# Performance work log

Measured on AMD Instinct MI355X. Metric: run time of the kernel, lower is better.

The kernel has to match this reference:

```python
import jax, jax.numpy as jnp
import numpy as np

B, M, E, R = 4, 72, 24, 552          # docs, mentions/doc, entities/doc, pairs/doc
L, H, A = 1024, 1024, 16             # seq_len, hidden (LUKE-large), attn heads
EMB, BLK, OUT, NC = 768, 64, 768, 97 # embed_size, block_size, out_embed_size, num_class


def setup_inputs() -> dict:
    key = jax.random.key(0)
    ks = jax.random.split(key, 12)
    s = 0.02  # weight scale to keep tanh unsaturated
    return {
        "seq_lhs": jax.random.normal(ks[0], (B, L, H), jnp.float32),
        "ent_lhs": jax.random.normal(ks[1], (B, M, H), jnp.float32),
        "ent_to_seq_attn": jax.random.uniform(ks[2], (B, A, M, L), jnp.float32),
        "entity_id_labels": jax.random.randint(ks[3], (B, M), 0, E, jnp.int32),
        "hts": jax.random.randint(ks[4], (B, R, 2), 0, E, jnp.int32),
        "W_head": jax.random.normal(ks[5], (2 * H, EMB), jnp.float32) * s,
        "b_head": jnp.zeros((EMB,), jnp.float32),
        "W_tail": jax.random.normal(ks[6], (2 * H, EMB), jnp.float32) * s,
        "b_tail": jnp.zeros((EMB,), jnp.float32),
        "W_bil": jax.random.normal(ks[7], (EMB * BLK, OUT), jnp.float32) * s,
        "b_bil": jnp.zeros((OUT,), jnp.float32),
        "W_cls": jax.random.normal(ks[8], (OUT, NC), jnp.float32) * s,
        "b_cls": jnp.zeros((NC,), jnp.float32),
        "W_bin": jax.random.normal(ks[9], (OUT, 1), jnp.float32) * s,
        "b_bin": jnp.zeros((1,), jnp.float32),
    }


def _hrt_pool(seq_lhs, ent_lhs, ent_to_seq_attn, entity_id_labels, hts):
    # global segment id: doc_i * E + entity_label  -> [B*M]
    seg = (jnp.arange(B, dtype=entity_id_labels.dtype)[:, None] * E
           + entity_id_labels).reshape(-1)
    NSEG = B * E

    # --- entity embedding: logsumexp over mentions of each entity (0 if empty) ---
    x = ent_lhs.reshape(B * M, H)
    mx = jax.ops.segment_max(x, seg, num_segments=NSEG)          # -inf for empty
    mx_safe = jnp.where(jnp.isfinite(mx), mx, 0.0)
    ssum = jax.ops.segment_sum(jnp.exp(x - mx_safe[seg]), seg, num_segments=NSEG)
    cnt = jax.ops.segment_sum(jnp.ones((B * M,), x.dtype), seg, num_segments=NSEG)
    ent_emb = jnp.where(cnt[:, None] > 0, jnp.log(ssum) + mx_safe, 0.0)
    ent_emb = ent_emb.reshape(B, E, H)

    # --- entity-to-seq attention: mean over mentions (0 if empty) ---
    a = ent_to_seq_attn.transpose(0, 2, 1, 3).reshape(B * M, A, L)
    asum = jax.ops.segment_sum(a, seg, num_segments=NSEG)
    amean = jnp.where(cnt[:, None, None] > 0,
                      asum / jnp.maximum(cnt, 1.0)[:, None, None], 0.0)
    amean = amean.reshape(B, E, A, L)

    # --- gather head/tail per pair ---
    bidx = jnp.arange(B)[:, None]
    hs = ent_emb[bidx, hts[:, :, 0]]       # [B,R,H]
    ts = ent_emb[bidx, hts[:, :, 1]]
    ha = amean[bidx, hts[:, :, 0]]         # [B,R,A,L]
    ta = amean[bidx, hts[:, :, 1]]

    ht_attn = (ha * ta).mean(axis=2)       # [B,R,L] mean over heads
    ht_attn = ht_attn / (ht_attn.sum(axis=-1, keepdims=True) + 1e-5)
    rel = jnp.einsum('bld,brl->brd', seq_lhs, ht_attn)  # [B,R,H]
    return hs, ts, rel


def reference(seq_lhs, ent_lhs, ent_to_seq_attn, entity_id_labels, hts,
              W_head, b_head, W_tail, b_tail, W_bil, b_bil,
              W_cls, b_cls, W_bin, b_bin):
    hs, ts, rel = _hrt_pool(seq_lhs, ent_lhs, ent_to_seq_attn,
                            entity_id_labels, hts)
    N = B * R
    hs = jnp.tanh(jnp.concatenate([hs, rel], -1).reshape(N, 2 * H) @ W_head + b_head)
    ts = jnp.tanh(jnp.concatenate([ts, rel], -1).reshape(N, 2 * H) @ W_tail + b_tail)

    K = EMB // BLK
    b1 = hs.reshape(N, K, BLK)
    b2 = ts.reshape(N, K, BLK)
    bl = (b1[:, :, :, None] * b2[:, :, None, :]).reshape(N, EMB * BLK)
    embeds = bl @ W_bil + b_bil                    # [N, OUT]
    class_logits = embeds @ W_cls + b_cls          # [N, NC]
    binary_logits = embeds @ W_bin + b_bin         # [N, 1]
    return embeds, class_logits, binary_logits
```

## Files before the change

kernel.cpp:

```cpp
#include <hip/hip_runtime.h>
#include <hip/hip_bf16.h>
#include <math.h>
#include <stdint.h>

#define B_ 4
#define M_ 72
#define E_ 24
#define R_ 552
#define L_ 1024
#define H_ 1024
#define A_ 16
#define EMB_ 768
#define BLK_ 64
#define OUT_ 768
#define NC_ 97
#define N_ (B_*R_)
#define NPAD_ 2304
#define K2H_ (2*H_)
#define KB_ (EMB_/BLK_)
#define KTOT_ (EMB_*BLK_)
#define SLICE2_ 524288

typedef short s16x8 __attribute__((ext_vector_type(8)));
typedef float f32x4 __attribute__((ext_vector_type(4)));
typedef uint32_t u32x4 __attribute__((ext_vector_type(4)));

__device__ __forceinline__ uint32_t pkbf16(float lo, float hi) {
    uint32_t r;
    asm("v_cvt_pk_bf16_f32 %0, %1, %2" : "=v"(r) : "v"(lo), "v"(hi));
    return r;
}
__device__ __forceinline__ unsigned short f2bf(float f) {
    uint32_t u = __builtin_bit_cast(uint32_t, f);
    uint32_t r = (u + 0x7fffu + ((u >> 16) & 1u)) >> 16;
    return (unsigned short)r;
}
__device__ __forceinline__ float bff(unsigned short u) {
    return __builtin_bit_cast(float, (uint32_t)u << 16);
}
__device__ __forceinline__ void gload_lds16(const void* g, void* l) {
    __builtin_amdgcn_global_load_lds(
        (const __attribute__((address_space(1))) unsigned int*)g,
        (__attribute__((address_space(3))) unsigned int*)l, 16, 0, 0);
}

__global__ void k_pool(const float* __restrict__ ent_lhs,
                       const float* __restrict__ attn,
                       const int*   __restrict__ labels,
                       unsigned short* __restrict__ ent_bf,
                       unsigned short* __restrict__ amean_bf)
{
    int b = blockIdx.x / E_;
    int e = blockIdx.x % E_;
    __shared__ int mlist[M_];
    __shared__ int mcount;
    if (threadIdx.x == 0) {
        int c = 0;
        for (int m = 0; m < M_; ++m)
            if (labels[b*M_ + m] == e) mlist[c++] = m;
        mcount = c;
    }
    __syncthreads();
    int cnt = mcount;

    for (int h = threadIdx.x; h < H_; h += blockDim.x) {
        float out = 0.f;
        if (cnt > 0) {
            float mx = -INFINITY;
            for (int q = 0; q < cnt; ++q)
                mx = fmaxf(mx, ent_lhs[(size_t)(b*M_ + mlist[q])*H_ + h]);
            float s = 0.f;
            for (int q = 0; q < cnt; ++q)
                s += expf(ent_lhs[(size_t)(b*M_ + mlist[q])*H_ + h] - mx);
            out = logf(s) + mx;
        }
        ent_bf[(size_t)(b*E_ + e)*H_ + h] = f2bf(out);
    }

    float inv = (cnt > 0) ? (1.f / (float)cnt) : 0.f;
    for (int c4 = threadIdx.x; c4 < A_*(L_/4); c4 += blockDim.x) {
        int a = c4 / (L_/4), l4 = c4 % (L_/4);
        float sx = 0.f, sy = 0.f, sz = 0.f, sw = 0.f;
        for (int q = 0; q < cnt; ++q) {
            float4 v = *(const float4*)(attn + ((size_t)(b*A_ + a)*M_ + mlist[q])*L_ + l4*4);
            sx += v.x; sy += v.y; sz += v.z; sw += v.w;
        }
        ushort4 o;
        o.x = f2bf(sx*inv); o.y = f2bf(sy*inv); o.z = f2bf(sz*inv); o.w = f2bf(sw*inv);
        *(ushort4*)(amean_bf + ((size_t)(b*E_ + e)*A_ + a)*L_ + l4*4) = o;
    }
}

__global__ void k_htattn(const unsigned short* __restrict__ amean_bf,
                         const int* __restrict__ hts,
                         unsigned short* __restrict__ htw_bf)
{
    int br = blockIdx.x;
    int b  = br / R_;
    int hh = hts[br*2 + 0], tt = hts[br*2 + 1];
    const unsigned short* pa = amean_bf + (size_t)(b*E_ + hh)*A_*L_;
    const unsigned short* pb = amean_bf + (size_t)(b*E_ + tt)*A_*L_;

    int l0 = threadIdx.x * 4;
    float v[4] = {0.f, 0.f, 0.f, 0.f};
    for (int a = 0; a < A_; ++a) {
        ushort4 ua = *(const ushort4*)(pa + (size_t)a*L_ + l0);
        ushort4 ub = *(const ushort4*)(pb + (size_t)a*L_ + l0);
        v[0] += bff(ua.x)*bff(ub.x); v[1] += bff(ua.y)*bff(ub.y);
        v[2] += bff(ua.z)*bff(ub.z); v[3] += bff(ua.w)*bff(ub.w);
    }
    float part = (v[0]+v[1]+v[2]+v[3]) * 0.0625f;
    __shared__ float red[256];
    red[threadIdx.x] = part;
    __syncthreads();
    for (int st = 128; st > 0; st >>= 1) {
        if (threadIdx.x < st) red[threadIdx.x] += red[threadIdx.x + st];
        __syncthreads();
    }
    float norm = 0.0625f / (red[0] + 1e-5f);
    unsigned short* po = htw_bf + (size_t)br*L_ + l0;
    po[0] = f2bf(v[0]*norm); po[1] = f2bf(v[1]*norm);
    po[2] = f2bf(v[2]*norm); po[3] = f2bf(v[3]*norm);
}

__global__ void k_transcvt(const float* __restrict__ W, unsigned short* __restrict__ Wt,
                           int K, int O)
{
    const float* src = W + (size_t)blockIdx.z*K*O;
    unsigned short* dst = Wt + (size_t)blockIdx.z*K*O;
    __shared__ unsigned short t[64][72];
    int k0 = blockIdx.x * 64, o0 = blockIdx.y * 64;
    #pragma unroll
    for (int p = 0; p < 16; ++p) {
        int idx = p*256 + threadIdx.x;
        int r = idx >> 6, c = idx & 63;
        t[c][r] = f2bf(src[(size_t)(k0 + r)*O + o0 + c]);
    }
    __syncthreads();
    #pragma unroll
    for (int p = 0; p < 16; ++p) {
        int idx = p*256 + threadIdx.x;
        int r = idx >> 6, c = idx & 63;
        dst[(size_t)(o0 + r)*K + k0 + c] = t[r][c];
    }
}

__global__ void k_cvtW2(const float* __restrict__ W, unsigned short* __restrict__ W2)
{
    __shared__ unsigned short t[64][72];
    int k0 = blockIdx.x * 64, o0 = blockIdx.y * 64;
    #pragma unroll
    for (int p = 0; p < 16; ++p) {
        int idx = p*256 + threadIdx.x;
        int r = idx >> 6, c = idx & 63;
        t[c][r] = f2bf(W[(size_t)(k0 + r)*OUT_ + o0 + c]);
    }
    __syncthreads();
    int kb = k0 >> 12;
    int i  = (k0 >> 6) & 63;
    int ob = o0 >> 7;
    int wc = (o0 >> 6) & 1;
    unsigned short* base = W2 + (size_t)(kb*6 + ob)*SLICE2_ + i*8192 + wc*4096;
    #pragma unroll
    for (int p = 0; p < 16; ++p) {
        int lin = p*256 + threadIdx.x;
        int e = lin & 7;
        int lane = (lin >> 3) & 63;
        int f = lin >> 9;
        int jh = f >> 2, ofl = f & 3;
        int j = (jh*4 + (lane >> 4))*8 + e;
        int o_local = ofl*16 + (lane & 15);
        base[f*512 + lane*8 + e] = t[o_local][j];
    }
}

__global__ void k_cvtWcat(const float* __restrict__ Wc, const float* __restrict__ Wbn,
                          unsigned short* __restrict__ WcatT)
{
    int idx = blockIdx.x*256 + threadIdx.x;
    if (idx < 256*768) {
        int o = idx / 768, k = idx % 768;
        float v = 0.f;
        if (o < NC_) v = Wc[(size_t)k*NC_ + o];
        else if (o == NC_) v = Wbn[k];
        WcatT[idx] = f2bf(v);
    }
}

__global__ __launch_bounds__(256, 2)
void k_rel_mfma(const unsigned short* __restrict__ htw,
                const unsigned short* __restrict__ seqT,
                unsigned short* __restrict__ rel_bf)
{
    int bid = blockIdx.x;
    int ot = bid & 7;
    int rest = bid >> 3;
    int mt = rest % 5;
    int b  = rest / 5;
    int m0 = mt*128, o0 = ot*128;
    int tid = threadIdx.x, lane = tid & 63, wid = tid >> 6;
    int wr = wid >> 1, wc = wid & 1;
    __shared__ __align__(16) unsigned short a_s[128*64];
    __shared__ __align__(16) unsigned short b_s[128*64];
    const unsigned short* Ab = htw + (size_t)b*R_*L_;
    const unsigned short* Bb = seqT + (size_t)b*H_*L_;

    u32x4 aR[4], bR[4];
    auto loadA = [&](int st) {
        #pragma unroll
        for (int q = 0; q < 4; ++q) {
            int slot = q*256 + tid;
            int r = slot >> 3, s = slot & 7;
            int ar = m0 + r; if (ar > R_-1) ar = R_-1;
            aR[q] = *(const u32x4*)(Ab + (size_t)ar*L_ + st*64 + s*8);
        }
    };
    auto loadB = [&](int st) {
        #pragma unroll
        for (int q = 0; q < 4; ++q) {
            int slot = q*256 + tid;
            int o = slot >> 3, s = slot & 7;
            bR[q] = *(const u32x4*)(Bb + (size_t)(o0+o)*L_ + st*64 + s*8);
        }
    };

    f32x4 acc[4][4];
    const f32x4 zz = {0.f,0.f,0.f,0.f};
    #pragma unroll
    for (int mf = 0; mf < 4; ++mf)
        #pragma unroll
        for (int of = 0; of < 4; ++of) acc[mf][of] = zz;

    loadA(0); loadB(0);
    for (int st = 0; st < 16; ++st) {
        __syncthreads();
        #pragma unroll
        for (int q = 0; q < 4; ++q) {
            int slot = q*256 + tid; int r = slot >> 3, s = slot & 7;
            *(u32x4*)((char*)a_s + r*128 + ((s ^ (r & 7)) << 4)) = aR[q];
        }
        #pragma unroll
        for (int q = 0; q < 4; ++q) {
            int slot = q*256 + tid; int o = slot >> 3, s = slot & 7;
            *(u32x4*)((char*)b_s + o*128 + ((s ^ (o & 7)) << 4)) = bR[q];
        }
        __syncthreads();
        if (st < 15) { loadA(st+1); loadB(st+1); }
        #pragma unroll
        for (int kh = 0; kh < 2; ++kh) {
            s16x8 af[4];
            #pragma unroll
            for (int mf = 0; mf < 4; ++mf) {
                int r = wr*64 + mf*16 + (lane & 15);
                int s = kh*4 + (lane >> 4);
                af[mf] = *(const s16x8*)((const char*)a_s + r*128 + ((s ^ (r & 7)) << 4));
            }
            #pragma unroll
            for (int of = 0; of < 4; ++of) {
                int ol = wc*64 + of*16 + (lane & 15);
                int s = kh*4 + (lane >> 4);
                s16x8 bfr = *(const s16x8*)((const char*)b_s + ol*128 + ((s ^ (ol & 7)) << 4));
                #pragma unroll
                for (int mf = 0; mf < 4; ++mf)
                    acc[mf][of] = __builtin_amdgcn_mfma_f32_16x16x32_bf16(
                        af[mf], bfr, acc[mf][of], 0, 0, 0);
            }
        }
    }
    #pragma unroll
    for (int mf = 0; mf < 4; ++mf)
        #pragma unroll
        for (int of = 0; of < 4; ++of) {
            int col = o0 + wc*64 + of*16 + (lane & 15);
            #pragma unroll
            for (int rr = 0; rr < 4; ++rr) {
                int row = m0 + wr*64 + mf*16 + (lane >> 4)*4 + rr;
                if (row < R_)
                    rel_bf[((size_t)b*R_ + row)*H_ + col] = f2bf(acc[mf][of][rr]);
            }
        }
}

__global__ void k_pinit(const float* __restrict__ b_head,
                        const float* __restrict__ b_tail,
                        float* __restrict__ pacc)
{
    int idx = blockIdx.x * 256 + threadIdx.x;
    if (idx < 2*NPAD_*OUT_) {
        const float* bb = (idx < NPAD_*OUT_) ? b_head : b_tail;
        pacc[idx] = bb[idx % OUT_];
    }
}

__global__ __launch_bounds__(256, 2)
void k_proj_mfma(const unsigned short* __restrict__ ent_bf,
                 const unsigned short* __restrict__ rel_bf,
                 const int* __restrict__ hts,
                 const unsigned short* __restrict__ Wph,
                 const unsigned short* __restrict__ Wpt,
                 float* __restrict__ pacc)
{
    int bid = blockIdx.x;
    int kq = bid & 3;
    int rest = bid >> 2;
    int ob = rest % 3;  rest /= 3;
    int mb = rest % 18;
    int which = rest / 18;
    int m0 = mb * 128, o0 = ob * 256;
    const unsigned short* Wp = which ? Wpt : Wph;
    float* out = pacc + (size_t)which*NPAD_*OUT_;
    int tid = threadIdx.x, lane = tid & 63, wid = tid >> 6;
    int wr = wid >> 1, wc = wid & 1;
    __shared__ __align__(16) unsigned short a_s[128*64];
    __shared__ __align__(16) unsigned short b_s[256*64];

    bool enthalf = (kq < 2);
    const unsigned short* abase[4];
    #pragma unroll
    for (int q = 0; q < 4; ++q) {
        int slot = q*256 + tid;
        int r = slot >> 3;
        int n = m0 + r;
        int nn = (n < N_) ? n : (N_ - 1);
        if (enthalf) {
            int bb = nn / R_;
            abase[q] = ent_bf + (size_t)(bb*E_ + hts[nn*2 + which])*H_ + kq*512;
        } else {
            abase[q] = rel_bf + (size_t)nn*H_ + (kq - 2)*512;
        }
    }
    u32x4 aR[4], bR[8];
    auto loadA = [&](int st) {
        #pragma unroll
        for (int q = 0; q < 4; ++q) {
            int s = (q*256 + tid) & 7;
            aR[q] = *(const u32x4*)(abase[q] + st*64 + s*8);
        }
    };
    auto loadB = [&](int st) {
        #pragma unroll
        for (int q = 0; q < 8; ++q) {
            int slot = q*256 + tid;
            int o = slot >> 3, s = slot & 7;
            bR[q] = *(const u32x4*)(Wp + (size_t)(o0+o)*K2H_ + kq*512 + st*64 + s*8);
        }
    };

    f32x4 acc[4][8];
    const f32x4 zz = {0.f,0.f,0.f,0.f};
    #pragma unroll
    for (int mf = 0; mf < 4; ++mf)
        #pragma unroll
        for (int of = 0; of < 8; ++of) acc[mf][of] = zz;

    loadA(0); loadB(0);
    for (int st = 0; st < 8; ++st) {
        __syncthreads();
        #pragma unroll
        for (int q = 0; q < 4; ++q) {
            int slot = q*256 + tid; int r = slot >> 3, s = slot & 7;
            *(u32x4*)((char*)a_s + r*128 + ((s ^ (r & 7)) << 4)) = aR[q];
        }
        #pragma unroll
        for (int q = 0; q < 8; ++q) {
            int slot = q*256 + tid; int o = slot >> 3, s = slot & 7;
            *(u32x4*)((char*)b_s + o*128 + ((s ^ (o & 7)) << 4)) = bR[q];
        }
        __syncthreads();
        if (st < 7) { loadA(st+1); loadB(st+1); }
        #pragma unroll
        for (int kh = 0; kh < 2; ++kh) {
            s16x8 af[4];
            #pragma unroll
            for (int mf = 0; mf < 4; ++mf) {
                int r = wr*64 + mf*16 + (lane & 15);
                int s = kh*4 + (lane >> 4);
                af[mf] = *(const s16x8*)((const char*)a_s + r*128 + ((s ^ (r & 7)) << 4));
            }
            #pragma unroll
            for (int of = 0; of < 8; ++of) {
                int ol = wc*128 + of*16 + (lane & 15);
                int s = kh*4 + (lane >> 4);
                s16x8 bfr = *(const s16x8*)((const char*)b_s + ol*128 + ((s ^ (ol & 7)) << 4));
                #pragma unroll
                for (int mf = 0; mf < 4; ++mf)
                    acc[mf][of] = __builtin_amdgcn_mfma_f32_16x16x32_bf16(
                        af[mf], bfr, acc[mf][of], 0, 0, 0);
            }
        }
    }
    #pragma unroll
    for (int mf = 0; mf < 4; ++mf)
        #pragma unroll
        for (int of = 0; of < 8; ++of) {
            int col = o0 + wc*128 + of*16 + (lane & 15);
            #pragma unroll
            for (int rr = 0; rr < 4; ++rr) {
                int row = m0 + wr*64 + mf*16 + (lane >> 4)*4 + rr;
                atomicAdd(&out[(size_t)row*OUT_ + col], acc[mf][of][rr]);
            }
        }
}

__global__ void k_tanhcvt(const float* __restrict__ pacc,
                          unsigned short* __restrict__ hsp,
                          unsigned short* __restrict__ tsp)
{
    int idx = blockIdx.x * 256 + threadIdx.x;
    if (idx < NPAD_*OUT_) {
        hsp[idx] = f2bf(tanhf(pacc[idx]));
        tsp[idx] = f2bf(tanhf(pacc[NPAD_*OUT_ + idx]));
    }
}

__global__ void k_bias_init(const float* __restrict__ bias, float* __restrict__ embeds)
{
    int idx = blockIdx.x * 256 + threadIdx.x;
    if (idx < N_*OUT_) embeds[idx] = bias[idx % OUT_];
}

__global__ __launch_bounds__(256, 2)
void k_bilinear_mfma(const unsigned short* __restrict__ hsp,
                     const unsigned short* __restrict__ tsp,
                     const unsigned short* __restrict__ W2,
                     float* __restrict__ embeds)
{
    int bid = blockIdx.x;
    int x = bid & 7, rest = bid >> 3;
    int g = rest / 18, mb = rest % 18;
    int s = g*8 + x;
    int kb = s / 6, ob = s % 6;
    int m0 = mb * 128;
    int tid = threadIdx.x, lane = tid & 63, wid = tid >> 6;
    int wr = wid >> 1, wc = wid & 1;

    __shared__ __align__(16) unsigned short hs_s[128*64];
    __shared__ __align__(16) unsigned short ts_s[128*64];

    #pragma unroll
    for (int q = 0; q < 4; ++q) {
        int slot = q*256 + tid;
        int r = slot >> 3, s7 = slot & 7;
        int gg = s7 ^ (r & 7);
        size_t srcoff = (size_t)(m0 + r)*EMB_ + kb*64 + (gg << 3);
        gload_lds16(hsp + srcoff, (char*)hs_s + (q*4096 + wid*1024));
        gload_lds16(tsp + srcoff, (char*)ts_s + (q*4096 + wid*1024));
    }
    __syncthreads();

    float tsf[4][2][8];
    #pragma unroll
    for (int mf = 0; mf < 4; ++mf) {
        int r = wr*64 + mf*16 + (lane & 15);
        #pragma unroll
        for (int jh = 0; jh < 2; ++jh) {
            int s8 = jh*4 + (lane >> 4);
            u32x4 tv = *(const u32x4*)((const char*)ts_s + r*128 + ((s8 ^ (r & 7)) << 4));
            #pragma unroll
            for (int p = 0; p < 4; ++p) {
                tsf[mf][jh][2*p]   = __builtin_bit_cast(float, tv[p] << 16);
                tsf[mf][jh][2*p+1] = __builtin_bit_cast(float, tv[p] & 0xffff0000u);
            }
        }
    }

    const unsigned short* Wsl = W2 + (size_t)s * SLICE2_ + wc*4096 + lane*8;

    f32x4 acc[4][4];
    const f32x4 zz = {0.f, 0.f, 0.f, 0.f};
    #pragma unroll
    for (int mf = 0; mf < 4; ++mf)
        #pragma unroll
        for (int of = 0; of < 4; ++of) acc[mf][of] = zz;

    u32x4 bA[8], bB[8];
    auto loadB = [&](int i, u32x4 (&buf)[8]) {
        const unsigned short* src = Wsl + (size_t)i*8192;
        #pragma unroll
        for (int f = 0; f < 8; ++f)
            buf[f] = *(const u32x4*)(src + f*512);
    };
    auto compute = [&](int i, u32x4 (&buf)[8]) {
        float hsf[4];
        #pragma unroll
        for (int mf = 0; mf < 4; ++mf) {
            int r = wr*64 + mf*16 + (lane & 15);
            int hb = r*128 + ((((i >> 3)) ^ (r & 7)) << 4) + (i & 7)*2;
            hsf[mf] = bff(*(const unsigned short*)((const char*)hs_s + hb));
        }
        #pragma unroll
        for (int jh = 0; jh < 2; ++jh) {
            s16x8 afr[4];
            #pragma unroll
            for (int mf = 0; mf < 4; ++mf) {
                u32x4 a;
                #pragma unroll
                for (int p = 0; p < 4; ++p)
                    a[p] = pkbf16(hsf[mf]*tsf[mf][jh][2*p], hsf[mf]*tsf[mf][jh][2*p+1]);
                afr[mf] = __builtin_bit_cast(s16x8, a);
            }
            #pragma unroll
            for (int of = 0; of < 4; ++of) {
                s16x8 bfr = __builtin_bit_cast(s16x8, buf[jh*4 + of]);
                #pragma unroll
                for (int mf = 0; mf < 4; ++mf)
                    acc[mf][of] = __builtin_amdgcn_mfma_f32_16x16x32_bf16(
                        afr[mf], bfr, acc[mf][of], 0, 0, 0);
            }
        }
    };

    loadB(0, bA);
    for (int i2 = 0; i2 < 32; ++i2) {
        loadB(2*i2 + 1, bB);
        compute(2*i2, bA);
        if (i2 < 31) loadB(2*i2 + 2, bA);
        compute(2*i2 + 1, bB);
    }

    #pragma unroll
    for (int mf = 0; mf < 4; ++mf) {
        #pragma unroll
        for (int of = 0; of < 4; ++of) {
            int col = ob*128 + wc*64 + of*16 + (lane & 15);
            #pragma unroll
            for (int rr = 0; rr < 4; ++rr) {
                int row = wr*64 + mf*16 + (lane >> 4)*4 + rr;
                int n = m0 + row;
                if (n < N_)
                    atomicAdd(&embeds[(size_t)n*OUT_ + col], acc[mf][of][rr]);
            }
        }
    }
}

__global__ void k_cvtemb(const float* __restrict__ embeds, unsigned short* __restrict__ emb_bf)
{
    int idx = blockIdx.x * 256 + threadIdx.x;
    if (idx < N_*OUT_) emb_bf[idx] = f2bf(embeds[idx]);
}

__global__ __launch_bounds__(256, 2)
void k_logits_mfma(const unsigned short* __restrict__ emb_bf,
                   const unsigned short* __restrict__ WcatT,
                   const float* __restrict__ bc, const float* __restrict__ bbn,
                   float* __restrict__ cls, float* __restrict__ bin)
{
    int m0 = blockIdx.x * 128;
    int tid = threadIdx.x, lane = tid & 63, wid = tid >> 6;
    int wr = wid >> 1, wc = wid & 1;
    __shared__ __align__(16) unsigned short a_s[128*64];
    __shared__ __align__(16) unsigned short b_s[256*64];

    u32x4 aR[4], bR[8];
    auto loadA = [&](int st) {
        #pragma unroll
        for (int q = 0; q < 4; ++q) {
            int slot = q*256 + tid;
            int r = slot >> 3, s = slot & 7;
            int ar = m0 + r; if (ar > N_-1) ar = N_-1;
            aR[q] = *(const u32x4*)(emb_bf + (size_t)ar*OUT_ + st*64 + s*8);
        }
    };
    auto loadB = [&](int st) {
        #pragma unroll
        for (int q = 0; q < 8; ++q) {
            int slot = q*256 + tid;
            int o = slot >> 3, s = slot & 7;
            bR[q] = *(const u32x4*)(WcatT + (size_t)o*OUT_ + st*64 + s*8);
        }
    };

    f32x4 acc[4][8];
    const f32x4 zz = {0.f,0.f,0.f,0.f};
    #pragma unroll
    for (int mf = 0; mf < 4; ++mf)
        #pragma unroll
        for (int of = 0; of < 8; ++of) acc[mf][of] = zz;

    loadA(0); loadB(0);
    for (int st = 0; st < 12; ++st) {
        __syncthreads();
        #pragma unroll
        for (int q = 0; q < 4; ++q) {
            int slot = q*256 + tid; int r = slot >> 3, s = slot & 7;
            *(u32x4*)((char*)a_s + r*128 + ((s ^ (r & 7)) << 4)) = aR[q];
        }
        #pragma unroll
        for (int q = 0; q < 8; ++q) {
            int slot = q*256 + tid; int o = slot >> 3, s = slot & 7;
            *(u32x4*)((char*)b_s + o*128 + ((s ^ (o & 7)) << 4)) = bR[q];
        }
        __syncthreads();
        if (st < 11) { loadA(st+1); loadB(st+1); }
        #pragma unroll
        for (int kh = 0; kh < 2; ++kh) {
            s16x8 af[4];
            #pragma unroll
            for (int mf = 0; mf < 4; ++mf) {
                int r = wr*64 + mf*16 + (lane & 15);
                int s = kh*4 + (lane >> 4);
                af[mf] = *(const s16x8*)((const char*)a_s + r*128 + ((s ^ (r & 7)) << 4));
            }
            #pragma unroll
            for (int of = 0; of < 8; ++of) {
                int ol = wc*128 + of*16 + (lane & 15);
                int s = kh*4 + (lane >> 4);
                s16x8 bfr = *(const s16x8*)((const char*)b_s + ol*128 + ((s ^ (ol & 7)) << 4));
                #pragma unroll
                for (int mf = 0; mf < 4; ++mf)
                    acc[mf][of] = __builtin_amdgcn_mfma_f32_16x16x32_bf16(
                        af[mf], bfr, acc[mf][of], 0, 0, 0);
            }
        }
    }
    #pragma unroll
    for (int mf = 0; mf < 4; ++mf)
        #pragma unroll
        for (int of = 0; of < 8; ++of) {
            int col = wc*128 + of*16 + (lane & 15);
            if (col <= NC_) {
                #pragma unroll
                for (int rr = 0; rr < 4; ++rr) {
                    int row = m0 + wr*64 + mf*16 + (lane >> 4)*4 + rr;
                    if (row < N_) {
                        float v = acc[mf][of][rr];
                        if (col < NC_) cls[(size_t)row*NC_ + col] = v + bc[col];
                        else           bin[row] = v + bbn[0];
                    }
                }
            }
        }
}

extern "C" void kernel_launch(void* const* d_in, const int* in_sizes, int n_in,
                              void* d_out, int out_size, void* d_ws, size_t ws_size,
                              hipStream_t stream) {
    const float* seq_lhs = (const float*)d_in[0];
    const float* ent_lhs = (const float*)d_in[1];
    const float* attn    = (const float*)d_in[2];
    const int*   labels  = (const int*)d_in[3];
    const int*   hts     = (const int*)d_in[4];
    const float* W_head  = (const float*)d_in[5];
    const float* b_head  = (const float*)d_in[6];
    const float* W_tail  = (const float*)d_in[7];
    const float* b_tail  = (const float*)d_in[8];
    const float* W_bil   = (const float*)d_in[9];
    const float* b_bil   = (const float*)d_in[10];
    const float* W_cls   = (const float*)d_in[11];
    const float* b_cls   = (const float*)d_in[12];
    const float* W_bin   = (const float*)d_in[13];
    const float* b_bin   = (const float*)d_in[14];

    float* out_embeds = (float*)d_out;
    float* out_cls    = out_embeds + (size_t)N_*OUT_;
    float* out_bin    = out_cls + (size_t)N_*NC_;

    float* ws = (float*)d_ws;
    size_t off = 0;
    unsigned short* ent_bf   = (unsigned short*)(ws + off); off += (size_t)B_*E_*H_/2;
    float* pacc = ws + off;
    unsigned short* amean_bf = (unsigned short*)(ws + off); off += (size_t)B_*E_*A_*L_/2;
    unsigned short* htw_bf   = (unsigned short*)(ws + off); off += (size_t)B_*R_*L_/2;
    unsigned short* seqT     = (unsigned short*)(ws + off); off += (size_t)B_*H_*L_/2;
    unsigned short* rel_bf   = (unsigned short*)(ws + off); off += (size_t)N_*H_/2;
    unsigned short* hsp      = (unsigned short*)(ws + off); off += (size_t)NPAD_*EMB_/2;
    unsigned short* tsp      = (unsigned short*)(ws + off); off += (size_t)NPAD_*EMB_/2;
    unsigned short* W2       = (unsigned short*)(ws + off); off += (size_t)OUT_*KTOT_/2;
    unsigned short* Wph      = (unsigned short*)(ws + off); off += (size_t)OUT_*K2H_/2;
    unsigned short* Wpt      = (unsigned short*)(ws + off); off += (size_t)OUT_*K2H_/2;
    unsigned short* WcatT    = (unsigned short*)(ws + off); off += (size_t)256*768/2;
    unsigned short* emb_bf   = (unsigned short*)(ws + off); off += (size_t)N_*OUT_/2;

    k_cvtW2<<<dim3(KTOT_/64, OUT_/64), 256, 0, stream>>>(W_bil, W2);
    k_transcvt<<<dim3(K2H_/64, OUT_/64, 1), 256, 0, stream>>>(W_head, Wph, K2H_, OUT_);
    k_transcvt<<<dim3(K2H_/64, OUT_/64, 1), 256, 0, stream>>>(W_tail, Wpt, K2H_, OUT_);
    k_transcvt<<<dim3(L_/64, H_/64, B_), 256, 0, stream>>>(seq_lhs, seqT, L_, H_);
    k_cvtWcat<<<(256*768)/256, 256, 0, stream>>>(W_cls, W_bin, WcatT);

    k_pool<<<B_*E_, 256, 0, stream>>>(ent_lhs, attn, labels, ent_bf, amean_bf);
    k_htattn<<<B_*R_, 256, 0, stream>>>(amean_bf, hts, htw_bf);
    k_rel_mfma<<<160, 256, 0, stream>>>(htw_bf, seqT, rel_bf);

    k_pinit<<<(2*NPAD_*OUT_ + 255)/256, 256, 0, stream>>>(b_head, b_tail, pacc);
    k_proj_mfma<<<2*18*3*4, 256, 0, stream>>>(ent_bf, rel_bf, hts, Wph, Wpt, pacc);
    k_tanhcvt<<<(NPAD_*OUT_ + 255)/256, 256, 0, stream>>>(pacc, hsp, tsp);

    k_bias_init<<<(N_*OUT_ + 255)/256, 256, 0, stream>>>(b_bil, out_embeds);
    k_bilinear_mfma<<<1296, 256, 0, stream>>>(hsp, tsp, W2, out_embeds);

    k_cvtemb<<<(N_*OUT_ + 255)/256, 256, 0, stream>>>(out_embeds, emb_bf);
    k_logits_mfma<<<18, 256, 0, stream>>>(emb_bf, WcatT, b_cls, b_bin,
                                          out_cls, out_bin);
}
```

Before: 475.2 us.

## Factor hs out of bilinear MFMA: multiply ts by W, then scale by hs

The bilinear kernel no longer builds the hs⊗ts outer-product A fragments in registers. For each hs index it runs MFMAs of raw ts against the W slice into a temporary, then scales the partial result by hs per output row in FP32 and adds it to the accumulator. hs is staged in LDS as a transposed fp32 array so a row-group's hs values come from one vector read. Per-element bf16 packing and multiplies on the A side go away, but VALU FMAs are added after each MFMA pair and the MFMAs now form dependent chains with fresh zero accumulators. The occupancy hint is also raised from 2 to 3 blocks.

```diff
diff --git a/kernel.cpp b/kernel.cpp
--- a/kernel.cpp
+++ b/kernel.cpp
@@ -419,7 +419,7 @@
     if (idx < N_*OUT_) embeds[idx] = bias[idx % OUT_];
 }
 
-__global__ __launch_bounds__(256, 2)
+__global__ __launch_bounds__(256, 3)
 void k_bilinear_mfma(const unsigned short* __restrict__ hsp,
                      const unsigned short* __restrict__ tsp,
                      const unsigned short* __restrict__ W2,
@@ -434,7 +434,7 @@
     int tid = threadIdx.x, lane = tid & 63, wid = tid >> 6;
     int wr = wid >> 1, wc = wid & 1;
 
-    __shared__ __align__(16) unsigned short hs_s[128*64];
+    __shared__ __align__(16) float hs_t[64*128];
     __shared__ __align__(16) unsigned short ts_s[128*64];
 
     #pragma unroll
@@ -443,28 +443,34 @@
         int r = slot >> 3, s7 = slot & 7;
         int gg = s7 ^ (r & 7);
         size_t srcoff = (size_t)(m0 + r)*EMB_ + kb*64 + (gg << 3);
-        gload_lds16(hsp + srcoff, (char*)hs_s + (q*4096 + wid*1024));
         gload_lds16(tsp + srcoff, (char*)ts_s + (q*4096 + wid*1024));
     }
+    #pragma unroll
+    for (int q = 0; q < 4; ++q) {
+        int slot = q*256 + tid;
+        int r = slot >> 3, s7 = slot & 7;
+        u32x4 v = *(const u32x4*)(hsp + (size_t)(m0 + r)*EMB_ + kb*64 + s7*8);
+        #pragma unroll
+        for (int p = 0; p < 4; ++p) {
+            hs_t[(s7*8 + 2*p    )*128 + r] = __builtin_bit_cast(float, v[p] << 16);
+            hs_t[(s7*8 + 2*p + 1)*128 + r] = __builtin_bit_cast(float, v[p] & 0xffff0000u);
+        }
+    }
     __syncthreads();
 
-    float tsf[4][2][8];
+    s16x8 tsr[4][2];
     #pragma unroll
     for (int mf = 0; mf < 4; ++mf) {
         int r = wr*64 + mf*16 + (lane & 15);
         #pragma unroll
         for (int jh = 0; jh < 2; ++jh) {
             int s8 = jh*4 + (lane >> 4);
-            u32x4 tv = *(const u32x4*)((const char*)ts_s + r*128 + ((s8 ^ (r & 7)) << 4));
-            #pragma unroll
-            for (int p = 0; p < 4; ++p) {
-                tsf[mf][jh][2*p]   = __builtin_bit_cast(float, tv[p] << 16);
-                tsf[mf][jh][2*p+1] = __builtin_bit_cast(float, tv[p] & 0xffff0000u);
-            }
+            tsr[mf][jh] = *(const s16x8*)((const char*)ts_s + r*128 + ((s8 ^ (r & 7)) << 4));
         }
     }
 
     const unsigned short* Wsl = W2 + (size_t)s * SLICE2_ + wc*4096 + lane*8;
+    int hrow4 = (lane >> 4)*4;
 
     f32x4 acc[4][4];
     const f32x4 zz = {0.f, 0.f, 0.f, 0.f};
@@ -481,31 +487,18 @@
             buf[f] = *(const u32x4*)(src + f*512);
     };
     auto compute = [&](int i, u32x4 (&buf)[8]) {
-        float hsf[4];
         #pragma unroll
         for (int mf = 0; mf < 4; ++mf) {
-            int r = wr*64 + mf*16 + (lane & 15);
-            int hb = r*128 + ((((i >> 3)) ^ (r & 7)) << 4) + (i & 7)*2;
-            hsf[mf] = bff(*(const unsigned short*)((const char*)hs_s + hb));
-        }
-        #pragma unroll
-        for (int jh = 0; jh < 2; ++jh) {
-            s16x8 afr[4];
-            #pragma unroll
-            for (int mf = 0; mf < 4; ++mf) {
-                u32x4 a;
+            f32x4 hv = *(const f32x4*)(hs_t + i*128 + wr*64 + mf*16 + hrow4);
+            #pragma unroll
+            for (int of = 0; of < 4; ++of) {
+                f32x4 p = __builtin_amdgcn_mfma_f32_16x16x32_bf16(
+                    tsr[mf][0], __builtin_bit_cast(s16x8, buf[of]), zz, 0, 0, 0);
+                p = __builtin_amdgcn_mfma_f32_16x16x32_bf16(
+                    tsr[mf][1], __builtin_bit_cast(s16x8, buf[4 + of]), p, 0, 0, 0);
                 #pragma unroll
-                for (int p = 0; p < 4; ++p)
-                    a[p] = pkbf16(hsf[mf]*tsf[mf][jh][2*p], hsf[mf]*tsf[mf][jh][2*p+1]);
-                afr[mf] = __builtin_bit_cast(s16x8, a);
-            }
-            #pragma unroll
-            for (int of = 0; of < 4; ++of) {
-                s16x8 bfr = __builtin_bit_cast(s16x8, buf[jh*4 + of]);
-                #pragma unroll
-                for (int mf = 0; mf < 4; ++mf)
-                    acc[mf][of] = __builtin_amdgcn_mfma_f32_16x16x32_bf16(
-                        afr[mf], bfr, acc[mf][of], 0, 0, 0);
+                for (int rr = 0; rr < 4; ++rr)
+                    acc[mf][of][rr] += hv[rr] * p[rr];
             }
         }
     };
@@ -525,7 +518,7 @@
             int col = ob*128 + wc*64 + of*16 + (lane & 15);
             #pragma unroll
             for (int rr = 0; rr < 4; ++rr) {
-                int row = wr*64 + mf*16 + (lane >> 4)*4 + rr;
+                int row = wr*64 + mf*16 + hrow4 + rr;
                 int n = m0 + row;
                 if (n < N_)
                     atomicAdd(&embeds[(size_t)n*OUT_ + col], acc[mf][of][rr]);
```

Result: slower. 1.554 ms (+226.9%).
